# Kernel tuning notes

Measured on AMD Instinct MI355X. Metric: run time of the kernel, lower is better.

The kernel has to match this reference:

```python
import jax, jax.numpy as jnp
import numpy as np

D_MODEL = 256
N_HEADS = 8
D_K = D_MODEL // N_HEADS


def setup_inputs() -> dict:
    key = jax.random.key(0)
    ks = jax.random.split(key, 9)
    s = 1.0 / np.sqrt(D_MODEL)
    x = jax.random.normal(ks[0], (2, 4096, D_MODEL), dtype=jnp.float32)
    Wq = jax.random.uniform(ks[1], (D_MODEL, D_MODEL), minval=-s, maxval=s)
    bq = jax.random.uniform(ks[2], (D_MODEL,), minval=-s, maxval=s)
    Wk = jax.random.uniform(ks[3], (D_MODEL, D_MODEL), minval=-s, maxval=s)
    bk = jax.random.uniform(ks[4], (D_MODEL,), minval=-s, maxval=s)
    Wv = jax.random.uniform(ks[5], (D_MODEL, D_MODEL), minval=-s, maxval=s)
    bv = jax.random.uniform(ks[6], (D_MODEL,), minval=-s, maxval=s)
    Wo = jax.random.uniform(ks[7], (D_MODEL, D_MODEL), minval=-s, maxval=s)
    bo = jax.random.uniform(ks[8], (D_MODEL,), minval=-s, maxval=s)
    return {"q": x, "Wq": Wq, "bq": bq, "Wk": Wk, "bk": bk,
            "Wv": Wv, "bv": bv, "Wo": Wo, "bo": bo}


def reference(q, Wq, bq, Wk, bk, Wv, bv, Wo, bo):
    B, L, _ = q.shape
    # nn.Linear: y = x @ W.T + b ; weights stored as [out, in]
    Q = (jnp.einsum('bld,ed->ble', q, Wq) + bq).reshape(B, L, N_HEADS, D_K).transpose(0, 2, 1, 3)
    K = (jnp.einsum('bld,ed->ble', q, Wk) + bk).reshape(B, L, N_HEADS, D_K).transpose(0, 2, 1, 3)
    V = (jnp.einsum('bld,ed->ble', q, Wv) + bv).reshape(B, L, N_HEADS, D_K).transpose(0, 2, 1, 3)
    scores = jnp.einsum('bhqd,bhkd->bhqk', Q, K) / jnp.sqrt(jnp.float32(D_K))
    attn = jax.nn.softmax(scores, axis=-1)  # dropout p=0 (eval): identity
    out = jnp.einsum('bhqk,bhkd->bhqd', attn, V)
    out = out.transpose(0, 2, 1, 3).reshape(B, L, D_MODEL)
    return jnp.einsum('bld,ed->ble', out, Wo) + bo
```

## Files before the change

kernel.cpp:

```cpp
#include <hip/hip_runtime.h>

#define D_MODEL 256
#define NH 8
#define DK 32
#define SEQ 4096
#define BATCH 2
#define M_ROWS (BATCH * SEQ)
#define QSCALE 0.17677669529663687f

typedef __attribute__((ext_vector_type(8))) short bf16x8;
typedef __attribute__((ext_vector_type(4))) short s16x4;
typedef __attribute__((ext_vector_type(4))) float f32x4;
typedef __attribute__((ext_vector_type(16))) float f32x16;

template <int N> struct IC { static constexpr int v = N; };

static __device__ __forceinline__ short f2bf(float f) {
    unsigned u = __float_as_uint(f);
    u += 0x7fff + ((u >> 16) & 1);
    return (short)(u >> 16);
}

__global__ void cvt_kernel(const float* __restrict__ src, short* __restrict__ dst, int n4) {
    int i = blockIdx.x * blockDim.x + threadIdx.x;
    if (i >= n4) return;
    float4 v = reinterpret_cast<const float4*>(src)[i];
    s16x4 o;
    o.x = f2bf(v.x); o.y = f2bf(v.y); o.z = f2bf(v.z); o.w = f2bf(v.w);
    reinterpret_cast<s16x4*>(dst)[i] = o;
}

__global__ void cvtw_kernel(const float* __restrict__ W0, const float* __restrict__ W1,
                            const float* __restrict__ W2, const float* __restrict__ W3,
                            short* __restrict__ D0, short* __restrict__ D1,
                            short* __restrict__ D2, short* __restrict__ D3) {
    const int seg = blockIdx.x >> 6;
    const int i = (blockIdx.x & 63) * blockDim.x + threadIdx.x;
    const float* s = seg == 0 ? W0 : seg == 1 ? W1 : seg == 2 ? W2 : W3;
    short* d = seg == 0 ? D0 : seg == 1 ? D1 : seg == 2 ? D2 : D3;
    float4 v = reinterpret_cast<const float4*>(s)[i];
    s16x4 o;
    o.x = f2bf(v.x); o.y = f2bf(v.y); o.z = f2bf(v.z); o.w = f2bf(v.w);
    reinterpret_cast<s16x4*>(d)[i] = o;
}

template <int MODE>
__global__ __launch_bounds__(256) void gemm_kernel(
    const short* __restrict__ A,
    const short* __restrict__ W0, const short* __restrict__ W1, const short* __restrict__ W2,
    const float* __restrict__ b0, const float* __restrict__ b1, const float* __restrict__ b2,
    short* __restrict__ O0, short* __restrict__ O1, short* __restrict__ O2,
    float* __restrict__ Oout)
{
    const int ct = blockIdx.x;
    const int rt = blockIdx.y;
    const int tid = threadIdx.x;
    const int w = tid >> 6, l = tid & 63, l15 = l & 15, g = l >> 4;

    const short* W;
    const float* bias;
    short* dst = nullptr;
    int colbase;
    int mat = 0;
    if (MODE == 0) {
        mat = ct >> 2;
        colbase = (ct & 3) * 64;
        W = (mat == 0) ? W0 : (mat == 1) ? W1 : W2;
        bias = (mat == 0) ? b0 : (mat == 1) ? b1 : b2;
        dst = (mat == 0) ? O0 : (mat == 1) ? O1 : O2;
    } else {
        colbase = ct * 64;
        W = W0;
        bias = b0;
    }

    const int arow = rt * 64 + w * 16 + l15;
    f32x4 acc[4] = {};
#pragma unroll
    for (int ks = 0; ks < 8; ++ks) {
        bf16x8 a = *reinterpret_cast<const bf16x8*>(&A[arow * 256 + ks * 32 + 8 * g]);
#pragma unroll
        for (int c = 0; c < 4; ++c) {
            const int col = colbase + 16 * c + l15;
            bf16x8 bfr = *reinterpret_cast<const bf16x8*>(&W[col * 256 + ks * 32 + 8 * g]);
            acc[c] = __builtin_amdgcn_mfma_f32_16x16x32_bf16(a, bfr, acc[c], 0, 0, 0);
        }
    }

#pragma unroll
    for (int c = 0; c < 4; ++c) {
        const int col = colbase + 16 * c + l15;
        const float bv = bias[col];
#pragma unroll
        for (int r = 0; r < 4; ++r) {
            const int m = rt * 64 + w * 16 + 4 * g + r;
            float v = acc[c][r] + bv;
            if (MODE == 0) {
                const int hh = col >> 5, d = col & 31;
                const int bb = m >> 12, seq = m & 4095;
                if (mat == 0) v *= QSCALE;
                if (mat == 2) {
                    const int seqp = (seq & ~12) | ((seq & 4) << 1) | ((seq & 8) >> 1);
                    dst[((size_t)(bb * NH + hh) * DK + d) * SEQ + seqp] = f2bf(v);
                } else {
                    dst[(size_t)(bb * NH + hh) * (SEQ * DK) + (size_t)seq * DK + d] = f2bf(v);
                }
            } else {
                Oout[(size_t)m * 256 + col] = v;
            }
        }
    }
}

__global__ __launch_bounds__(128) void attn_kernel(
    const short* __restrict__ Qb, const short* __restrict__ Kb,
    const short* __restrict__ Vb, short* __restrict__ AOb)
{
    __shared__ __align__(16) short Klds[3][2048];
    __shared__ __align__(16) short Vlds[3][2048];
    __shared__ float Sinv[2][32];

    const int qt = blockIdx.x & 63;
    const int bh = blockIdx.x >> 6;
    const int b = bh >> 3, h = bh & 7;
    const int w = threadIdx.x >> 6;
    const int l = threadIdx.x & 63;
    const int l31 = l & 31, g1 = l >> 5;

    const short* Qh = Qb + (size_t)bh * SEQ * DK;
    const char* Kg = (const char*)(Kb + (size_t)bh * SEQ * DK);
    const char* Vg = (const char*)(Vb + (size_t)bh * DK * SEQ);

    const int q0 = qt * 64 + w * 32;
    const bf16x8 qf0 = *(const bf16x8*)&Qh[(size_t)(q0 + l31) * DK + g1 * 8];
    const bf16x8 qf1 = *(const bf16x8*)&Qh[(size_t)(q0 + l31) * DK + 16 + g1 * 8];

    const int krow0 = w * 32 + (l >> 2);
    const int kbk = l & 3;
    const long ksrc0 = (long)krow0 * 64 + ((kbk ^ (krow0 & 3)) << 4);
    const int krow1 = krow0 + 16;
    const long ksrc1 = (long)krow1 * 64 + ((kbk ^ (krow1 & 3)) << 4);
    const int vd0 = w * 16 + (l >> 3);
    const int vbk = l & 7;
    const long vsrc0 = (long)vd0 * 8192 + ((vbk ^ (vd0 & 7)) << 4);
    const int vd1 = vd0 + 8;
    const long vsrc1 = (long)vd1 * 8192 + ((vbk ^ (vd1 & 7)) << 4);

    int koff[2][2];
#pragma unroll
    for (int s = 0; s < 2; ++s)
#pragma unroll
        for (int hh = 0; hh < 2; ++hh)
            koff[s][hh] = (s * 32 + l31) * 64 + (((hh * 2 + g1) ^ (l31 & 3)) << 4);
    int voff[4];
#pragma unroll
    for (int c = 0; c < 4; ++c)
        voff[c] = l31 * 128 + (((2 * c + g1) ^ (l31 & 7)) << 4);

    f32x16 acc = {0.f,0.f,0.f,0.f,0.f,0.f,0.f,0.f,0.f,0.f,0.f,0.f,0.f,0.f,0.f,0.f};
    float ls0 = 0.f, ls1 = 0.f, ls2 = 0.f, ls3 = 0.f;

    auto stage = [&](int t, int bi) {
        const long tk = (long)t * 4096;
        const long tv = (long)t * 128;
        __builtin_amdgcn_global_load_lds(
            (const __attribute__((address_space(1))) void*)(Kg + tk + ksrc0),
            (__attribute__((address_space(3))) void*)&Klds[bi][w * 1024], 16, 0, 0);
        __builtin_amdgcn_global_load_lds(
            (const __attribute__((address_space(1))) void*)(Kg + tk + ksrc1),
            (__attribute__((address_space(3))) void*)&Klds[bi][w * 1024 + 512], 16, 0, 0);
        __builtin_amdgcn_global_load_lds(
            (const __attribute__((address_space(1))) void*)(Vg + tv + vsrc0),
            (__attribute__((address_space(3))) void*)&Vlds[bi][w * 1024], 16, 0, 0);
        __builtin_amdgcn_global_load_lds(
            (const __attribute__((address_space(1))) void*)(Vg + tv + vsrc1),
            (__attribute__((address_space(3))) void*)&Vlds[bi][w * 1024 + 512], 16, 0, 0);
    };

    auto compute = [&](auto bic) {
        constexpr int BI = decltype(bic)::v;
        unsigned pk[2][8];
#pragma unroll
        for (int s = 0; s < 2; ++s) {
            f32x16 z = {0.f,0.f,0.f,0.f,0.f,0.f,0.f,0.f,0.f,0.f,0.f,0.f,0.f,0.f,0.f,0.f};
#pragma unroll
            for (int hh = 0; hh < 2; ++hh) {
                bf16x8 kf = *(const bf16x8*)((const char*)&Klds[BI][0] + koff[s][hh]);
                z = __builtin_amdgcn_mfma_f32_32x32x16_bf16(kf, hh ? qf1 : qf0, z, 0, 0, 0);
            }
            float e[16];
#pragma unroll
            for (int r = 0; r < 16; ++r) e[r] = __expf(z[r]);
#pragma unroll
            for (int r = 0; r < 16; r += 4) {
                ls0 += e[r]; ls1 += e[r + 1]; ls2 += e[r + 2]; ls3 += e[r + 3];
            }
#pragma unroll
            for (int i = 0; i < 8; ++i)
                asm("v_cvt_pk_bf16_f32 %0, %1, %2" : "=v"(pk[s][i]) : "v"(e[2 * i]), "v"(e[2 * i + 1]));
        }
#pragma unroll
        for (int c = 0; c < 4; ++c) {
            union { unsigned u[4]; bf16x8 bv; } pa;
            pa.u[0] = pk[c >> 1][4 * (c & 1) + 0];
            pa.u[1] = pk[c >> 1][4 * (c & 1) + 1];
            pa.u[2] = pk[c >> 1][4 * (c & 1) + 2];
            pa.u[3] = pk[c >> 1][4 * (c & 1) + 3];
            bf16x8 vf = *(const bf16x8*)((const char*)&Vlds[BI][0] + voff[c]);
            acc = __builtin_amdgcn_mfma_f32_32x32x16_bf16(pa.bv, vf, acc, 0, 0, 0);
        }
    };

#define STEP(T, U)                                                     \
    {                                                                  \
        const int t_ = (T);                                            \
        asm volatile("s_waitcnt vmcnt(4)" ::: "memory");               \
        __builtin_amdgcn_s_barrier();                                  \
        asm volatile("" ::: "memory");                                 \
        if (t_ < 62) stage(t_ + 2, ((U) + 2) % 3);                     \
        compute(IC<(U)>{});                                            \
    }

    stage(0, 0);
    stage(1, 1);
    for (int tb = 0; tb < 63; tb += 3) {
        STEP(tb + 0, 0);
        STEP(tb + 1, 1);
        STEP(tb + 2, 2);
    }
    asm volatile("s_waitcnt vmcnt(0)" ::: "memory");
    __builtin_amdgcn_s_barrier();
    asm volatile("" ::: "memory");
    compute(IC<0>{});
#undef STEP

    float lsum = (ls0 + ls1) + (ls2 + ls3);
    lsum += __shfl_xor(lsum, 32);
    Sinv[w][l31] = 1.0f / lsum;
#pragma unroll
    for (int r = 0; r < 16; ++r) {
        const int ql = (r & 3) + 8 * (r >> 2) + 4 * g1;
        const float v = acc[r] * Sinv[w][ql];
        AOb[((size_t)b * SEQ + q0 + ql) * D_MODEL + h * DK + l31] = f2bf(v);
    }
}

extern "C" void kernel_launch(void* const* d_in, const int* in_sizes, int n_in,
                              void* d_out, int out_size, void* d_ws, size_t ws_size,
                              hipStream_t stream) {
    const float* x  = (const float*)d_in[0];
    const float* Wq = (const float*)d_in[1];
    const float* bq = (const float*)d_in[2];
    const float* Wk = (const float*)d_in[3];
    const float* bk = (const float*)d_in[4];
    const float* Wv = (const float*)d_in[5];
    const float* bv = (const float*)d_in[6];
    const float* Wo = (const float*)d_in[7];
    const float* bo = (const float*)d_in[8];
    float* out = (float*)d_out;

    char* ws = (char*)d_ws;
    const size_t MB = 1 << 20, KB = 1 << 10;
    short* xb  = (short*)(ws);
    short* Wqb = (short*)(ws + 4 * MB);
    short* Wkb = (short*)(ws + 4 * MB + 128 * KB);
    short* Wvb = (short*)(ws + 4 * MB + 256 * KB);
    short* Wob = (short*)(ws + 4 * MB + 384 * KB);
    short* Qb  = (short*)(ws + 4 * MB + 512 * KB);
    short* Kb  = (short*)(ws + 8 * MB + 512 * KB);
    short* Vtb = (short*)(ws + 12 * MB + 512 * KB);
    short* AOb = (short*)(ws + 16 * MB + 512 * KB);

    cvt_kernel<<<2048, 256, 0, stream>>>(x, xb, (M_ROWS * D_MODEL) / 4);
    cvtw_kernel<<<256, 256, 0, stream>>>(Wq, Wk, Wv, Wo, Wqb, Wkb, Wvb, Wob);

    dim3 gq(12, 128);
    gemm_kernel<0><<<gq, 256, 0, stream>>>(xb, Wqb, Wkb, Wvb, bq, bk, bv, Qb, Kb, Vtb, nullptr);

    attn_kernel<<<BATCH * NH * (SEQ / 64), 128, 0, stream>>>(Qb, Kb, Vtb, AOb);

    dim3 go(4, 128);
    gemm_kernel<1><<<go, 256, 0, stream>>>(AOb, Wob, nullptr, nullptr, bo, nullptr, nullptr,
                                           nullptr, nullptr, nullptr, out);
}
```

Measured before the change: 131.5 us.

## Pre-block K/V into MFMA fragment layout and load directly to registers

The QKV GEMM now writes K and V in a blocked layout matching the per-lane MFMA operand order, so the attention kernel can load fragments straight from global memory into registers with fully coalesced 16-byte loads. It drops LDS staging, barriers and the triple buffer, and instead double-buffers the tiles in registers. Each block is now a single wave handling 32 queries, with block IDs remapped so that concurrently running blocks share a head's K/V in cache. The cost is that every wave reloads K/V from L2 on its own rather than sharing it through LDS, and register pressure rises.

```diff
diff --git a/kernel.cpp b/kernel.cpp
--- a/kernel.cpp
+++ b/kernel.cpp
@@ -12,8 +12,6 @@
 typedef __attribute__((ext_vector_type(4))) short s16x4;
 typedef __attribute__((ext_vector_type(4))) float f32x4;
 typedef __attribute__((ext_vector_type(16))) float f32x16;
-
-template <int N> struct IC { static constexpr int v = N; };
 
 static __device__ __forceinline__ short f2bf(float f) {
     unsigned u = __float_as_uint(f);
@@ -44,150 +42,104 @@
     reinterpret_cast<s16x4*>(d)[i] = o;
 }
 
-template <int MODE>
-__global__ __launch_bounds__(256) void gemm_kernel(
+__global__ __launch_bounds__(256) void qkv_gemm(
     const short* __restrict__ A,
-    const short* __restrict__ W0, const short* __restrict__ W1, const short* __restrict__ W2,
-    const float* __restrict__ b0, const float* __restrict__ b1, const float* __restrict__ b2,
-    short* __restrict__ O0, short* __restrict__ O1, short* __restrict__ O2,
-    float* __restrict__ Oout)
+    const short* __restrict__ Wqb, const short* __restrict__ Wkb, const short* __restrict__ Wvb,
+    const float* __restrict__ bq, const float* __restrict__ bk, const float* __restrict__ bv,
+    short* __restrict__ Qb, short* __restrict__ Kblk, short* __restrict__ Vblk)
 {
     const int ct = blockIdx.x;
     const int rt = blockIdx.y;
     const int tid = threadIdx.x;
     const int w = tid >> 6, l = tid & 63, l15 = l & 15, g = l >> 4;
-
-    const short* W;
-    const float* bias;
-    short* dst = nullptr;
-    int colbase;
-    int mat = 0;
-    if (MODE == 0) {
-        mat = ct >> 2;
-        colbase = (ct & 3) * 64;
-        W = (mat == 0) ? W0 : (mat == 1) ? W1 : W2;
-        bias = (mat == 0) ? b0 : (mat == 1) ? b1 : b2;
-        dst = (mat == 0) ? O0 : (mat == 1) ? O1 : O2;
-    } else {
-        colbase = ct * 64;
-        W = W0;
-        bias = b0;
-    }
+    const int mat = ct >> 2;
+    const int colbase = (ct & 3) * 64;
+    const short* W = mat == 0 ? Wqb : mat == 1 ? Wkb : Wvb;
+    const float* bias = mat == 0 ? bq : mat == 1 ? bk : bv;
 
     const int arow = rt * 64 + w * 16 + l15;
     f32x4 acc[4] = {};
 #pragma unroll
     for (int ks = 0; ks < 8; ++ks) {
-        bf16x8 a = *reinterpret_cast<const bf16x8*>(&A[arow * 256 + ks * 32 + 8 * g]);
+        bf16x8 af = *reinterpret_cast<const bf16x8*>(&A[(size_t)arow * 256 + ks * 32 + 8 * g]);
 #pragma unroll
         for (int c = 0; c < 4; ++c) {
             const int col = colbase + 16 * c + l15;
-            bf16x8 bfr = *reinterpret_cast<const bf16x8*>(&W[col * 256 + ks * 32 + 8 * g]);
-            acc[c] = __builtin_amdgcn_mfma_f32_16x16x32_bf16(a, bfr, acc[c], 0, 0, 0);
+            bf16x8 wf = *reinterpret_cast<const bf16x8*>(&W[(size_t)col * 256 + ks * 32 + 8 * g]);
+            acc[c] = __builtin_amdgcn_mfma_f32_16x16x32_bf16(af, wf, acc[c], 0, 0, 0);
         }
     }
 
 #pragma unroll
     for (int c = 0; c < 4; ++c) {
         const int col = colbase + 16 * c + l15;
-        const float bv = bias[col];
+        const float bv_ = bias[col];
 #pragma unroll
         for (int r = 0; r < 4; ++r) {
             const int m = rt * 64 + w * 16 + 4 * g + r;
-            float v = acc[c][r] + bv;
-            if (MODE == 0) {
-                const int hh = col >> 5, d = col & 31;
-                const int bb = m >> 12, seq = m & 4095;
-                if (mat == 0) v *= QSCALE;
-                if (mat == 2) {
-                    const int seqp = (seq & ~12) | ((seq & 4) << 1) | ((seq & 8) >> 1);
-                    dst[((size_t)(bb * NH + hh) * DK + d) * SEQ + seqp] = f2bf(v);
-                } else {
-                    dst[(size_t)(bb * NH + hh) * (SEQ * DK) + (size_t)seq * DK + d] = f2bf(v);
-                }
+            const float v = acc[c][r] + bv_;
+            const int head = col >> 5, d = col & 31;
+            const int bb = m >> 12, seq = m & 4095;
+            const size_t bhbase = (size_t)(bb * NH + head) * (SEQ * DK);
+            if (mat == 0) {
+                Qb[bhbase + (size_t)seq * 32 + d] = f2bf(v * QSCALE);
+            } else if (mat == 1) {
+                const int t = seq >> 6, s = (seq >> 5) & 1, lk = seq & 31;
+                const int hh = (d >> 4) & 1, gk = (d >> 3) & 1, jk = d & 7;
+                Kblk[bhbase + t * 2048 + (s * 2 + hh) * 512 + (gk * 32 + lk) * 8 + jk] = f2bf(v);
             } else {
-                Oout[(size_t)m * 256 + col] = v;
+                const int t = seq >> 6, w6 = seq & 63;
+                const int c2 = w6 >> 4, gv = (w6 >> 2) & 1, jv = ((w6 >> 3) & 1) * 4 + (w6 & 3);
+                Vblk[bhbase + t * 2048 + c2 * 512 + (gv * 32 + d) * 8 + jv] = f2bf(v);
             }
         }
     }
 }
 
-__global__ __launch_bounds__(128) void attn_kernel(
-    const short* __restrict__ Qb, const short* __restrict__ Kb,
-    const short* __restrict__ Vb, short* __restrict__ AOb)
+__global__ __launch_bounds__(64) void attn_kernel(
+    const short* __restrict__ Qb, const short* __restrict__ Kblk,
+    const short* __restrict__ Vblk, short* __restrict__ AOb)
 {
-    __shared__ __align__(16) short Klds[3][2048];
-    __shared__ __align__(16) short Vlds[3][2048];
-    __shared__ float Sinv[2][32];
-
-    const int qt = blockIdx.x & 63;
-    const int bh = blockIdx.x >> 6;
+    const int bid = ((int)blockIdx.x & 7) * 256 + ((int)blockIdx.x >> 3);
+    const int qt = bid & 127;
+    const int bh = bid >> 7;
     const int b = bh >> 3, h = bh & 7;
-    const int w = threadIdx.x >> 6;
-    const int l = threadIdx.x & 63;
+    const int l = threadIdx.x;
     const int l31 = l & 31, g1 = l >> 5;
 
-    const short* Qh = Qb + (size_t)bh * SEQ * DK;
-    const char* Kg = (const char*)(Kb + (size_t)bh * SEQ * DK);
-    const char* Vg = (const char*)(Vb + (size_t)bh * DK * SEQ);
-
-    const int q0 = qt * 64 + w * 32;
-    const bf16x8 qf0 = *(const bf16x8*)&Qh[(size_t)(q0 + l31) * DK + g1 * 8];
-    const bf16x8 qf1 = *(const bf16x8*)&Qh[(size_t)(q0 + l31) * DK + 16 + g1 * 8];
-
-    const int krow0 = w * 32 + (l >> 2);
-    const int kbk = l & 3;
-    const long ksrc0 = (long)krow0 * 64 + ((kbk ^ (krow0 & 3)) << 4);
-    const int krow1 = krow0 + 16;
-    const long ksrc1 = (long)krow1 * 64 + ((kbk ^ (krow1 & 3)) << 4);
-    const int vd0 = w * 16 + (l >> 3);
-    const int vbk = l & 7;
-    const long vsrc0 = (long)vd0 * 8192 + ((vbk ^ (vd0 & 7)) << 4);
-    const int vd1 = vd0 + 8;
-    const long vsrc1 = (long)vd1 * 8192 + ((vbk ^ (vd1 & 7)) << 4);
-
-    int koff[2][2];
-#pragma unroll
-    for (int s = 0; s < 2; ++s)
-#pragma unroll
-        for (int hh = 0; hh < 2; ++hh)
-            koff[s][hh] = (s * 32 + l31) * 64 + (((hh * 2 + g1) ^ (l31 & 3)) << 4);
-    int voff[4];
-#pragma unroll
-    for (int c = 0; c < 4; ++c)
-        voff[c] = l31 * 128 + (((2 * c + g1) ^ (l31 & 7)) << 4);
-
-    f32x16 acc = {0.f,0.f,0.f,0.f,0.f,0.f,0.f,0.f,0.f,0.f,0.f,0.f,0.f,0.f,0.f,0.f};
+    const short* Qh = Qb + (size_t)bh * (SEQ * DK);
+    const int q0 = qt * 32;
+    const bf16x8 qf0 = *(const bf16x8*)&Qh[(size_t)(q0 + l31) * 32 + g1 * 8];
+    const bf16x8 qf1 = *(const bf16x8*)&Qh[(size_t)(q0 + l31) * 32 + 16 + g1 * 8];
+
+    const char* Kt = (const char*)Kblk + (size_t)bh * 262144 + l * 16;
+    const char* Vt = (const char*)Vblk + (size_t)bh * 262144 + l * 16;
+
+    f32x16 acc;
+#pragma unroll
+    for (int r = 0; r < 16; ++r) acc[r] = 0.f;
     float ls0 = 0.f, ls1 = 0.f, ls2 = 0.f, ls3 = 0.f;
 
-    auto stage = [&](int t, int bi) {
-        const long tk = (long)t * 4096;
-        const long tv = (long)t * 128;
-        __builtin_amdgcn_global_load_lds(
-            (const __attribute__((address_space(1))) void*)(Kg + tk + ksrc0),
-            (__attribute__((address_space(3))) void*)&Klds[bi][w * 1024], 16, 0, 0);
-        __builtin_amdgcn_global_load_lds(
-            (const __attribute__((address_space(1))) void*)(Kg + tk + ksrc1),
-            (__attribute__((address_space(3))) void*)&Klds[bi][w * 1024 + 512], 16, 0, 0);
-        __builtin_amdgcn_global_load_lds(
-            (const __attribute__((address_space(1))) void*)(Vg + tv + vsrc0),
-            (__attribute__((address_space(3))) void*)&Vlds[bi][w * 1024], 16, 0, 0);
-        __builtin_amdgcn_global_load_lds(
-            (const __attribute__((address_space(1))) void*)(Vg + tv + vsrc1),
-            (__attribute__((address_space(3))) void*)&Vlds[bi][w * 1024 + 512], 16, 0, 0);
+    auto loadt = [&](bf16x8& K0, bf16x8& K1, bf16x8& K2, bf16x8& K3,
+                     bf16x8& V0, bf16x8& V1, bf16x8& V2, bf16x8& V3, int tl) {
+        const char* kp = Kt + (size_t)tl * 4096;
+        const char* vp = Vt + (size_t)tl * 4096;
+        K0 = *(const bf16x8*)(kp);        K1 = *(const bf16x8*)(kp + 1024);
+        K2 = *(const bf16x8*)(kp + 2048); K3 = *(const bf16x8*)(kp + 3072);
+        V0 = *(const bf16x8*)(vp);        V1 = *(const bf16x8*)(vp + 1024);
+        V2 = *(const bf16x8*)(vp + 2048); V3 = *(const bf16x8*)(vp + 3072);
     };
 
-    auto compute = [&](auto bic) {
-        constexpr int BI = decltype(bic)::v;
+    auto compute = [&](const bf16x8& K0, const bf16x8& K1, const bf16x8& K2, const bf16x8& K3,
+                       const bf16x8& V0, const bf16x8& V1, const bf16x8& V2, const bf16x8& V3) {
         unsigned pk[2][8];
 #pragma unroll
         for (int s = 0; s < 2; ++s) {
-            f32x16 z = {0.f,0.f,0.f,0.f,0.f,0.f,0.f,0.f,0.f,0.f,0.f,0.f,0.f,0.f,0.f,0.f};
-#pragma unroll
-            for (int hh = 0; hh < 2; ++hh) {
-                bf16x8 kf = *(const bf16x8*)((const char*)&Klds[BI][0] + koff[s][hh]);
-                z = __builtin_amdgcn_mfma_f32_32x32x16_bf16(kf, hh ? qf1 : qf0, z, 0, 0, 0);
-            }
+            f32x16 z;
+#pragma unroll
+            for (int r = 0; r < 16; ++r) z[r] = 0.f;
+            z = __builtin_amdgcn_mfma_f32_32x32x16_bf16(s ? K2 : K0, qf0, z, 0, 0, 0);
+            z = __builtin_amdgcn_mfma_f32_32x32x16_bf16(s ? K3 : K1, qf1, z, 0, 0, 0);
             float e[16];
 #pragma unroll
             for (int r = 0; r < 16; ++r) e[r] = __expf(z[r]);
@@ -202,46 +154,64 @@
 #pragma unroll
         for (int c = 0; c < 4; ++c) {
             union { unsigned u[4]; bf16x8 bv; } pa;
-            pa.u[0] = pk[c >> 1][4 * (c & 1) + 0];
-            pa.u[1] = pk[c >> 1][4 * (c & 1) + 1];
-            pa.u[2] = pk[c >> 1][4 * (c & 1) + 2];
-            pa.u[3] = pk[c >> 1][4 * (c & 1) + 3];
-            bf16x8 vf = *(const bf16x8*)((const char*)&Vlds[BI][0] + voff[c]);
+#pragma unroll
+            for (int i = 0; i < 4; ++i) pa.u[i] = pk[c >> 1][4 * (c & 1) + i];
+            const bf16x8& vf = (c == 0) ? V0 : (c == 1) ? V1 : (c == 2) ? V2 : V3;
             acc = __builtin_amdgcn_mfma_f32_32x32x16_bf16(pa.bv, vf, acc, 0, 0, 0);
         }
     };
 
-#define STEP(T, U)                                                     \
-    {                                                                  \
-        const int t_ = (T);                                            \
-        asm volatile("s_waitcnt vmcnt(4)" ::: "memory");               \
-        __builtin_amdgcn_s_barrier();                                  \
-        asm volatile("" ::: "memory");                                 \
-        if (t_ < 62) stage(t_ + 2, ((U) + 2) % 3);                     \
-        compute(IC<(U)>{});                                            \
-    }
-
-    stage(0, 0);
-    stage(1, 1);
-    for (int tb = 0; tb < 63; tb += 3) {
-        STEP(tb + 0, 0);
-        STEP(tb + 1, 1);
-        STEP(tb + 2, 2);
-    }
-    asm volatile("s_waitcnt vmcnt(0)" ::: "memory");
-    __builtin_amdgcn_s_barrier();
-    asm volatile("" ::: "memory");
-    compute(IC<0>{});
-#undef STEP
-
-    float lsum = (ls0 + ls1) + (ls2 + ls3);
-    lsum += __shfl_xor(lsum, 32);
-    Sinv[w][l31] = 1.0f / lsum;
+    bf16x8 kA0, kA1, kA2, kA3, vA0, vA1, vA2, vA3;
+    bf16x8 kB0, kB1, kB2, kB3, vB0, vB1, vB2, vB3;
+    loadt(kA0, kA1, kA2, kA3, vA0, vA1, vA2, vA3, 0);
+    for (int i = 0; i < 32; ++i) {
+        loadt(kB0, kB1, kB2, kB3, vB0, vB1, vB2, vB3, 2 * i + 1);
+        compute(kA0, kA1, kA2, kA3, vA0, vA1, vA2, vA3);
+        if (i < 31) loadt(kA0, kA1, kA2, kA3, vA0, vA1, vA2, vA3, 2 * i + 2);
+        compute(kB0, kB1, kB2, kB3, vB0, vB1, vB2, vB3);
+    }
+
+    float ls = (ls0 + ls1) + (ls2 + ls3);
+    ls += __shfl_xor(ls, 32);
+    const float inv = 1.0f / ls;
+
 #pragma unroll
     for (int r = 0; r < 16; ++r) {
         const int ql = (r & 3) + 8 * (r >> 2) + 4 * g1;
-        const float v = acc[r] * Sinv[w][ql];
-        AOb[((size_t)b * SEQ + q0 + ql) * D_MODEL + h * DK + l31] = f2bf(v);
+        const float invq = __shfl(inv, ql);
+        AOb[((size_t)b * SEQ + q0 + ql) * D_MODEL + h * DK + l31] = f2bf(acc[r] * invq);
+    }
+}
+
+__global__ __launch_bounds__(256) void out_gemm(
+    const short* __restrict__ AOb, const short* __restrict__ Wob,
+    const float* __restrict__ bo, float* __restrict__ out)
+{
+    const int ct = blockIdx.x, rt = blockIdx.y;
+    const int tid = threadIdx.x;
+    const int w = tid >> 6, l = tid & 63, l15 = l & 15, g = l >> 4;
+    const int arow = rt * 64 + w * 16 + l15;
+
+    f32x4 acc[4] = {};
+#pragma unroll
+    for (int ks = 0; ks < 8; ++ks) {
+        bf16x8 af = *(const bf16x8*)&AOb[(size_t)arow * 256 + ks * 32 + 8 * g];
+#pragma unroll
+        for (int c = 0; c < 4; ++c) {
+            const int col = ct * 64 + 16 * c + l15;
+            bf16x8 wf = *(const bf16x8*)&Wob[(size_t)col * 256 + ks * 32 + 8 * g];
+            acc[c] = __builtin_amdgcn_mfma_f32_16x16x32_bf16(af, wf, acc[c], 0, 0, 0);
+        }
+    }
+#pragma unroll
+    for (int c = 0; c < 4; ++c) {
+        const int col = ct * 64 + 16 * c + l15;
+        const float bv_ = bo[col];
+#pragma unroll
+        for (int r = 0; r < 4; ++r) {
+            const int m = rt * 64 + w * 16 + 4 * g + r;
+            out[(size_t)m * 256 + col] = acc[c][r] + bv_;
+        }
     }
 }
 
@@ -261,25 +231,24 @@
 
     char* ws = (char*)d_ws;
     const size_t MB = 1 << 20, KB = 1 << 10;
-    short* xb  = (short*)(ws);
-    short* Wqb = (short*)(ws + 4 * MB);
-    short* Wkb = (short*)(ws + 4 * MB + 128 * KB);
-    short* Wvb = (short*)(ws + 4 * MB + 256 * KB);
-    short* Wob = (short*)(ws + 4 * MB + 384 * KB);
-    short* Qb  = (short*)(ws + 4 * MB + 512 * KB);
-    short* Kb  = (short*)(ws + 8 * MB + 512 * KB);
-    short* Vtb = (short*)(ws + 12 * MB + 512 * KB);
-    short* AOb = (short*)(ws + 16 * MB + 512 * KB);
+    short* xb   = (short*)(ws);
+    short* Wqb  = (short*)(ws + 4 * MB);
+    short* Wkb  = (short*)(ws + 4 * MB + 128 * KB);
+    short* Wvb  = (short*)(ws + 4 * MB + 256 * KB);
+    short* Wob  = (short*)(ws + 4 * MB + 384 * KB);
+    short* Qb   = (short*)(ws + 4 * MB + 512 * KB);
+    short* Kblk = (short*)(ws + 8 * MB + 512 * KB);
+    short* Vblk = (short*)(ws + 12 * MB + 512 * KB);
+    short* AOb  = (short*)(ws + 16 * MB + 512 * KB);
 
     cvt_kernel<<<2048, 256, 0, stream>>>(x, xb, (M_ROWS * D_MODEL) / 4);
     cvtw_kernel<<<256, 256, 0, stream>>>(Wq, Wk, Wv, Wo, Wqb, Wkb, Wvb, Wob);
 
     dim3 gq(12, 128);
-    gemm_kernel<0><<<gq, 256, 0, stream>>>(xb, Wqb, Wkb, Wvb, bq, bk, bv, Qb, Kb, Vtb, nullptr);
-
-    attn_kernel<<<BATCH * NH * (SEQ / 64), 128, 0, stream>>>(Qb, Kb, Vtb, AOb);
+    qkv_gemm<<<gq, 256, 0, stream>>>(xb, Wqb, Wkb, Wvb, bq, bk, bv, Qb, Kblk, Vblk);
+
+    attn_kernel<<<2048, 64, 0, stream>>>(Qb, Kblk, Vblk, AOb);
 
     dim3 go(4, 128);
-    gemm_kernel<1><<<go, 256, 0, stream>>>(AOb, Wob, nullptr, nullptr, bo, nullptr, nullptr,
-                                           nullptr, nullptr, nullptr, out);
-}
+    out_gemm<<<go, 256, 0, stream>>>(AOb, Wob, bo, out);
+}
```

New measurement: 116.2 us. 1.13x faster.
